# Kernel optimization log

Hardware: AMD Instinct MI355X
Metric: run time of the kernel (lower is better)

The kernel has to match this reference:

```python
import jax, jax.numpy as jnp
import numpy as np

EPS = 1e-5

def layer_norm(x, alpha, beta):
    mean = jnp.mean(x, axis=-1, keepdims=True)
    var = jnp.mean(jnp.square(x - mean), axis=-1, keepdims=True)
    return alpha * ((x - mean) / jnp.sqrt(var + EPS)) + beta

def setup_inputs() -> dict:
    key = jax.random.key(0)
    B, S, D, H = 4, 2048, 1024, 16
    Dff = 4 * D
    ks = jax.random.split(key, 8)
    inp = {
        "x": jax.random.normal(ks[0], (B, S, D), jnp.float32),
        "attention_mask": jnp.ones((B, S), jnp.int32),
        "ln1_alpha": jnp.ones((D,), jnp.float32),
        "ln1_beta": jnp.zeros((D,), jnp.float32),
        "ln2_alpha": jnp.ones((D,), jnp.float32),
        "ln2_beta": jnp.zeros((D,), jnp.float32),
        "Wq": jax.random.normal(ks[1], (D, D), jnp.float32) * 0.05,
        "Wk": jax.random.normal(ks[2], (D, D), jnp.float32) * 0.05,
        "Wv": jax.random.normal(ks[3], (D, D), jnp.float32) * 0.05,
        "Wo": jax.random.normal(ks[4], (D, D), jnp.float32) * 0.05,
        "W1": jax.random.normal(ks[5], (D, Dff), jnp.float32) * 0.02,
        "b1": jnp.zeros((Dff,), jnp.float32),
        "W2": jax.random.normal(ks[6], (Dff, D), jnp.float32) * 0.02,
        "b2": jnp.zeros((D,), jnp.float32),
    }
    return inp

def reference(x, attention_mask, ln1_alpha, ln1_beta, ln2_alpha, ln2_beta,
              Wq, Wk, Wv, Wo, W1, b1, W2, b2):
    B, S, D = x.shape
    H = 16
    dh = D // H

    # LN1 + self-attention
    y = layer_norm(x, ln1_alpha, ln1_beta)
    Q = (y @ Wq).reshape(B, S, H, dh).transpose(0, 2, 1, 3)  # [B,H,S,dh]
    K = (y @ Wk).reshape(B, S, H, dh).transpose(0, 2, 1, 3)
    V = (y @ Wv).reshape(B, S, H, dh).transpose(0, 2, 1, 3)

    scores = jnp.einsum("bhqd,bhkd->bhqk", Q, K) / jnp.sqrt(jnp.float32(dh))
    causal = jnp.tril(jnp.ones((S, S), jnp.float32))  # [S,S]
    tmask = attention_mask.astype(jnp.float32)  # [B,S]
    amask = causal[None, None, :, :] * tmask[:, None, None, :] * tmask[:, None, :, None]
    scores = jnp.where(amask > 0, scores, jnp.float32(-1e30))
    attn = jax.nn.softmax(scores, axis=-1)
    # dropout omitted (deterministic inference)
    ctx = jnp.einsum("bhqk,bhkd->bhqd", attn, V)
    ctx = ctx.transpose(0, 2, 1, 3).reshape(B, S, D)
    x = x + ctx @ Wo

    # LN2 + GELU FFN
    y = layer_norm(x, ln2_alpha, ln2_beta)
    h = jax.nn.gelu(y @ W1 + b1, approximate=False)
    x = x + (h @ W2 + b2)
    return x
```

## Files before the change

### kernel.cpp

```cpp
#include <hip/hip_runtime.h>
#include <math.h>

typedef unsigned short u16;
typedef unsigned int u32;
typedef __attribute__((ext_vector_type(4))) unsigned short u16x4;
typedef __attribute__((ext_vector_type(8))) short bf16x8;
typedef __attribute__((ext_vector_type(4))) float f32x4;

#define B_ 4
#define S_ 2048
#define D_ 1024
#define H_ 16
#define NT (B_*S_)
#define DFF 4096

static __device__ __forceinline__ float bf2f(u16 u) {
    return __uint_as_float(((u32)u) << 16);
}
static __device__ __forceinline__ u16 f2bf(float f) {
    u32 u = __float_as_uint(f);
    u32 r = (u + 0x7fffu + ((u >> 16) & 1u)) >> 16;
    return (u16)r;
}
static __device__ __forceinline__ void gload_lds16(const void* g, void* l) {
    __builtin_amdgcn_global_load_lds(
        (const __attribute__((address_space(1))) void*)g,
        (__attribute__((address_space(3))) void*)l, 16, 0, 0);
}
static __device__ __forceinline__ float gelu_fast(float x) {
    float x2 = x * x;
    float u = x * fmaf(0.044715f, x2, 1.0f);
    float e = exp2f(2.3022079f * u);
    float r = __builtin_amdgcn_rcpf(e + 1.0f);
    return x - x * r;
}

#define MBAR() do { asm volatile("" ::: "memory"); \
                    __builtin_amdgcn_s_barrier(); \
                    asm volatile("" ::: "memory"); } while (0)
#define SBAR0() __builtin_amdgcn_sched_barrier(0)

__global__ void transpose_f2b4(const float* __restrict__ s0, const float* __restrict__ s1,
                               const float* __restrict__ s2, const float* __restrict__ s3,
                               u16* __restrict__ d0, u16* __restrict__ d1,
                               u16* __restrict__ d2, u16* __restrict__ d3,
                               int R, int C) {
    const float* in = s0; u16* out = d0;
    if (blockIdx.z == 1) { in = s1; out = d1; }
    else if (blockIdx.z == 2) { in = s2; out = d2; }
    else if (blockIdx.z == 3) { in = s3; out = d3; }
    __shared__ float t[32][33];
    int c0 = blockIdx.x * 32, r0 = blockIdx.y * 32;
    int x = threadIdx.x, y = threadIdx.y;
    #pragma unroll
    for (int i = 0; i < 4; i++)
        t[y + i*8][x] = in[(long)(r0 + y + i*8) * C + c0 + x];
    __syncthreads();
    #pragma unroll
    for (int i = 0; i < 4; i++)
        out[(long)(c0 + y + i*8) * R + r0 + x] = f2bf(t[x][y + i*8]);
}

__global__ void transpose_f2b(const float* __restrict__ in, u16* __restrict__ out,
                              int R, int C) {
    __shared__ float t[32][33];
    int c0 = blockIdx.x * 32, r0 = blockIdx.y * 32;
    int x = threadIdx.x, y = threadIdx.y;
    #pragma unroll
    for (int i = 0; i < 4; i++)
        t[y + i*8][x] = in[(long)(r0 + y + i*8) * C + c0 + x];
    __syncthreads();
    #pragma unroll
    for (int i = 0; i < 4; i++)
        out[(long)(c0 + y + i*8) * R + r0 + x] = f2bf(t[x][y + i*8]);
}

__global__ void transpose_v(const u16* __restrict__ V, u16* __restrict__ Vt) {
    __shared__ u16 t[32][33];
    int z = blockIdx.z; int b = z >> 4, h = z & 15;
    int s0 = blockIdx.x * 32, d0 = blockIdx.y * 32;
    int x = threadIdx.x, y = threadIdx.y;
    const u16* in = V + ((long)b * S_ + s0) * D_ + h * 64 + d0;
    #pragma unroll
    for (int i = 0; i < 4; i++)
        t[y + i*8][x] = in[(long)(y + i*8) * D_ + x];
    __syncthreads();
    u16* out = Vt + ((long)z * 64 + d0) * S_ + s0;
    #pragma unroll
    for (int i = 0; i < 4; i++)
        out[(long)(y + i*8) * S_ + x] = t[x][y + i*8];
}

__global__ __launch_bounds__(256) void ln_kernel(
    const float* __restrict__ X, const float* __restrict__ alpha,
    const float* __restrict__ beta, u16* __restrict__ Y) {
    int row = blockIdx.x, tid = threadIdx.x;
    float4 xv = ((const float4*)(X + (long)row * D_))[tid];
    float v[4] = {xv.x, xv.y, xv.z, xv.w};
    float s = 0.f, ss = 0.f;
    #pragma unroll
    for (int i = 0; i < 4; i++) { s += v[i]; ss += v[i]*v[i]; }
    #pragma unroll
    for (int off = 32; off >= 1; off >>= 1) {
        s += __shfl_xor(s, off);
        ss += __shfl_xor(ss, off);
    }
    __shared__ float red[8];
    __shared__ float stats[2];
    int w = tid >> 6;
    if ((tid & 63) == 0) { red[w] = s; red[4 + w] = ss; }
    __syncthreads();
    if (tid == 0) {
        float S = red[0] + red[1] + red[2] + red[3];
        float SS = red[4] + red[5] + red[6] + red[7];
        float mean = S * (1.f / D_);
        float var = SS * (1.f / D_) - mean * mean;
        stats[0] = mean; stats[1] = rsqrtf(var + 1e-5f);
    }
    __syncthreads();
    float mean = stats[0], rstd = stats[1];
    float4 av = ((const float4*)alpha)[tid];
    float4 bv = ((const float4*)beta)[tid];
    u16x4 o;
    o[0] = f2bf((v[0] - mean) * rstd * av.x + bv.x);
    o[1] = f2bf((v[1] - mean) * rstd * av.y + bv.y);
    o[2] = f2bf((v[2] - mean) * rstd * av.z + bv.z);
    o[3] = f2bf((v[3] - mean) * rstd * av.w + bv.w);
    *(u16x4*)(Y + (long)row * D_ + tid * 4) = o;
}

#define BM2 256
#define BN2 256
#define BK2 64

__global__ __launch_bounds__(512, 2) void gemm8p(
    const u16* __restrict__ A, const u16* __restrict__ Bt,
    u16* __restrict__ C0, u16* __restrict__ C1, u16* __restrict__ C2,
    int N, int K, int mode, const float* __restrict__ bias) {
    __shared__ __align__(16) u16 lds[2 * 32768];

    int tid = threadIdx.x;
    int lane = tid & 63, wave = tid >> 6;
    int l15 = lane & 15, quad = lane >> 4;
    int wm = wave & 1, wn = wave >> 1;
    long tm0 = (long)blockIdx.y * BM2, tn0 = (long)blockIdx.x * BN2;
    int srow = lane >> 3;
    int scolw = ((lane & 7) ^ srow) * 8;
    int sk = l15 & 7;
    int ca0 = ((quad) ^ sk) * 8;
    int ca1 = ((4 + quad) ^ sk) * 8;
    int steps = K >> 6;

    auto STAGE = [&](int kt, int half, int buf) {
        long kk = (long)kt * BK2;
        #pragma unroll
        for (int c = 0; c < 2; c++) {
            int chunk = wave * 2 + c;
            int rloc = (half & 1) * 128 + chunk * 8 + srow;
            const u16* g = (half < 2)
                ? &A [(tm0 + rloc) * (long)K + kk + scolw]
                : &Bt[(tn0 + rloc) * (long)K + kk + scolw];
            u16* l = &lds[buf * 32768 + (half >= 2 ? 16384 : 0)
                          + (half & 1) * 8192 + chunk * 512];
            gload_lds16(g, l);
        }
    };

    f32x4 acc[8][4] = {};
    bf16x8 af[4][2], bl[2][2], bh[2][2];

    STAGE(0, 0, 0); STAGE(0, 1, 0); STAGE(0, 2, 0); STAGE(0, 3, 0);
    if (steps > 1) { STAGE(1, 2, 1); STAGE(1, 3, 1); }
    if (steps > 1) asm volatile("s_waitcnt vmcnt(4)" ::: "memory");
    else           asm volatile("s_waitcnt vmcnt(0)" ::: "memory");
    MBAR();

    for (int t = 0; t < steps; ++t) {
        int cur = t & 1;
        const u16* Ab = &lds[cur * 32768];
        const u16* Bb = &lds[cur * 32768 + 16384];
        bool pf1 = (t + 1 < steps), pf2 = (t + 2 < steps);

        #pragma unroll
        for (int mt = 0; mt < 4; mt++) {
            int row = wm*128 + mt*16 + l15;
            af[mt][0] = *(const bf16x8*)&Ab[row * BK2 + ca0];
            af[mt][1] = *(const bf16x8*)&Ab[row * BK2 + ca1];
        }
        #pragma unroll
        for (int nt = 0; nt < 2; nt++) {
            int row = wn*64 + nt*16 + l15;
            bl[nt][0] = *(const bf16x8*)&Bb[row * BK2 + ca0];
            bl[nt][1] = *(const bf16x8*)&Bb[row * BK2 + ca1];
        }
        if (pf1) STAGE(t + 1, 0, cur ^ 1);
        MBAR();
        SBAR0();
        __builtin_amdgcn_s_setprio(1);
        #pragma unroll
        for (int mt = 0; mt < 4; mt++)
            #pragma unroll
            for (int nt = 0; nt < 2; nt++) {
                acc[mt][nt] = __builtin_amdgcn_mfma_f32_16x16x32_bf16(af[mt][0], bl[nt][0], acc[mt][nt], 0,0,0);
                acc[mt][nt] = __builtin_amdgcn_mfma_f32_16x16x32_bf16(af[mt][1], bl[nt][1], acc[mt][nt], 0,0,0);
            }
        __builtin_amdgcn_s_setprio(0);
        SBAR0();
        MBAR();

        #pragma unroll
        for (int nt = 0; nt < 2; nt++) {
            int row = wn*64 + (2+nt)*16 + l15;
            bh[nt][0] = *(const bf16x8*)&Bb[row * BK2 + ca0];
            bh[nt][1] = *(const bf16x8*)&Bb[row * BK2 + ca1];
        }
        if (pf1) STAGE(t + 1, 1, cur ^ 1);
        MBAR();
        SBAR0();
        __builtin_amdgcn_s_setprio(1);
        #pragma unroll
        for (int mt = 0; mt < 4; mt++)
            #pragma unroll
            for (int nt = 0; nt < 2; nt++) {
                acc[mt][2+nt] = __builtin_amdgcn_mfma_f32_16x16x32_bf16(af[mt][0], bh[nt][0], acc[mt][2+nt], 0,0,0);
                acc[mt][2+nt] = __builtin_amdgcn_mfma_f32_16x16x32_bf16(af[mt][1], bh[nt][1], acc[mt][2+nt], 0,0,0);
            }
        __builtin_amdgcn_s_setprio(0);
        SBAR0();
        MBAR();

        #pragma unroll
        for (int mt = 0; mt < 4; mt++) {
            int row = wm*128 + 64 + mt*16 + l15;
            af[mt][0] = *(const bf16x8*)&Ab[row * BK2 + ca0];
            af[mt][1] = *(const bf16x8*)&Ab[row * BK2 + ca1];
        }
        if (pf2) STAGE(t + 2, 2, cur);
        MBAR();
        SBAR0();
        __builtin_amdgcn_s_setprio(1);
        #pragma unroll
        for (int mt = 0; mt < 4; mt++)
            #pragma unroll
            for (int nt = 0; nt < 2; nt++) {
                acc[4+mt][2+nt] = __builtin_amdgcn_mfma_f32_16x16x32_bf16(af[mt][0], bh[nt][0], acc[4+mt][2+nt], 0,0,0);
                acc[4+mt][2+nt] = __builtin_amdgcn_mfma_f32_16x16x32_bf16(af[mt][1], bh[nt][1], acc[4+mt][2+nt], 0,0,0);
            }
        __builtin_amdgcn_s_setprio(0);
        SBAR0();
        MBAR();

        if (pf2) STAGE(t + 2, 3, cur);
        MBAR();
        SBAR0();
        __builtin_amdgcn_s_setprio(1);
        #pragma unroll
        for (int mt = 0; mt < 4; mt++)
            #pragma unroll
            for (int nt = 0; nt < 2; nt++) {
                acc[4+mt][nt] = __builtin_amdgcn_mfma_f32_16x16x32_bf16(af[mt][0], bl[nt][0], acc[4+mt][nt], 0,0,0);
                acc[4+mt][nt] = __builtin_amdgcn_mfma_f32_16x16x32_bf16(af[mt][1], bl[nt][1], acc[4+mt][nt], 0,0,0);
            }
        __builtin_amdgcn_s_setprio(0);
        SBAR0();
        if (pf2) asm volatile("s_waitcnt vmcnt(4)" ::: "memory");
        else     asm volatile("s_waitcnt vmcnt(0)" ::: "memory");
        MBAR();
    }

    #pragma unroll
    for (int mt = 0; mt < 8; mt++) {
        #pragma unroll
        for (int nt = 0; nt < 4; nt++) {
            #pragma unroll
            for (int i = 0; i < 4; i++) {
                long r = tm0 + wm*128 + mt*16 + quad*4 + i;
                int cn = (int)tn0 + wn*64 + nt*16 + l15;
                float val = acc[mt][nt][i];
                if (mode == 0) {
                    int mi = cn >> 10;
                    int col = cn & 1023;
                    u16* base = (mi == 0) ? C0 : (mi == 1 ? C1 : C2);
                    base[r * 1024 + col] = f2bf(val);
                } else {
                    val += bias[cn];
                    C0[r * (long)N + cn] = f2bf(gelu_fast(val));
                }
            }
        }
    }
}

__global__ __launch_bounds__(512, 2) void gemm8p_n128(
    const u16* __restrict__ A, const u16* __restrict__ Bt,
    float* __restrict__ C, int N, int K,
    const float* __restrict__ bias, const float* __restrict__ resid) {
    __shared__ __align__(16) u16 lds[2 * 24576];

    int tid = threadIdx.x;
    int lane = tid & 63, wave = tid >> 6;
    int l15 = lane & 15, quad = lane >> 4;
    int wm = wave & 1, wn = wave >> 1;
    long tm0 = (long)blockIdx.y * 256, tn0 = (long)blockIdx.x * 128;
    int srow = lane >> 3;
    int scolw = ((lane & 7) ^ srow) * 8;
    int sk = l15 & 7;
    int ca0 = ((quad) ^ sk) * 8;
    int ca1 = ((4 + quad) ^ sk) * 8;
    int steps = K >> 6;

    auto STAGE = [&](int kt, int half, int buf) {
        long kk = (long)kt * 64;
        if (half < 2) {
            #pragma unroll
            for (int c = 0; c < 2; c++) {
                int chunk = wave * 2 + c;
                int rloc = half * 128 + chunk * 8 + srow;
                gload_lds16(&A[(tm0 + rloc) * (long)K + kk + scolw],
                            &lds[buf * 24576 + half * 8192 + chunk * 512]);
            }
        } else {
            int rloc = (half - 2) * 64 + wave * 8 + srow;
            gload_lds16(&Bt[(tn0 + rloc) * (long)K + kk + scolw],
                        &lds[buf * 24576 + 16384 + (half - 2) * 4096 + wave * 512]);
        }
    };

    f32x4 acc[8][2] = {};
    bf16x8 af[4][2], bl[2], bh[2];

    STAGE(0, 0, 0); STAGE(0, 1, 0); STAGE(0, 2, 0); STAGE(0, 3, 0);
    if (steps > 1) { STAGE(1, 2, 1); STAGE(1, 3, 1); }
    if (steps > 1) asm volatile("s_waitcnt vmcnt(2)" ::: "memory");
    else           asm volatile("s_waitcnt vmcnt(0)" ::: "memory");
    MBAR();

    for (int t = 0; t < steps; ++t) {
        int cur = t & 1;
        const u16* Ab = &lds[cur * 24576];
        const u16* Bb = &lds[cur * 24576 + 16384];
        bool pf1 = (t + 1 < steps), pf2 = (t + 2 < steps);

        #pragma unroll
        for (int mt = 0; mt < 4; mt++) {
            int row = wm*128 + mt*16 + l15;
            af[mt][0] = *(const bf16x8*)&Ab[row * 64 + ca0];
            af[mt][1] = *(const bf16x8*)&Ab[row * 64 + ca1];
        }
        {
            int row = wn*32 + l15;
            bl[0] = *(const bf16x8*)&Bb[row * 64 + ca0];
            bl[1] = *(const bf16x8*)&Bb[row * 64 + ca1];
        }
        if (pf1) STAGE(t + 1, 0, cur ^ 1);
        MBAR();
        SBAR0();
        __builtin_amdgcn_s_setprio(1);
        #pragma unroll
        for (int mt = 0; mt < 4; mt++) {
            acc[mt][0] = __builtin_amdgcn_mfma_f32_16x16x32_bf16(af[mt][0], bl[0], acc[mt][0], 0,0,0);
            acc[mt][0] = __builtin_amdgcn_mfma_f32_16x16x32_bf16(af[mt][1], bl[1], acc[mt][0], 0,0,0);
        }
        __builtin_amdgcn_s_setprio(0);
        SBAR0();
        MBAR();

        {
            int row = wn*32 + 16 + l15;
            bh[0] = *(const bf16x8*)&Bb[row * 64 + ca0];
            bh[1] = *(const bf16x8*)&Bb[row * 64 + ca1];
        }
        if (pf1) STAGE(t + 1, 1, cur ^ 1);
        MBAR();
        SBAR0();
        __builtin_amdgcn_s_setprio(1);
        #pragma unroll
        for (int mt = 0; mt < 4; mt++) {
            acc[mt][1] = __builtin_amdgcn_mfma_f32_16x16x32_bf16(af[mt][0], bh[0], acc[mt][1], 0,0,0);
            acc[mt][1] = __builtin_amdgcn_mfma_f32_16x16x32_bf16(af[mt][1], bh[1], acc[mt][1], 0,0,0);
        }
        __builtin_amdgcn_s_setprio(0);
        SBAR0();
        MBAR();

        #pragma unroll
        for (int mt = 0; mt < 4; mt++) {
            int row = wm*128 + 64 + mt*16 + l15;
            af[mt][0] = *(const bf16x8*)&Ab[row * 64 + ca0];
            af[mt][1] = *(const bf16x8*)&Ab[row * 64 + ca1];
        }
        if (pf2) STAGE(t + 2, 2, cur);
        MBAR();
        SBAR0();
        __builtin_amdgcn_s_setprio(1);
        #pragma unroll
        for (int mt = 0; mt < 4; mt++) {
            acc[4+mt][1] = __builtin_amdgcn_mfma_f32_16x16x32_bf16(af[mt][0], bh[0], acc[4+mt][1], 0,0,0);
            acc[4+mt][1] = __builtin_amdgcn_mfma_f32_16x16x32_bf16(af[mt][1], bh[1], acc[4+mt][1], 0,0,0);
        }
        __builtin_amdgcn_s_setprio(0);
        SBAR0();
        MBAR();

        if (pf2) STAGE(t + 2, 3, cur);
        MBAR();
        SBAR0();
        __builtin_amdgcn_s_setprio(1);
        #pragma unroll
        for (int mt = 0; mt < 4; mt++) {
            acc[4+mt][0] = __builtin_amdgcn_mfma_f32_16x16x32_bf16(af[mt][0], bl[0], acc[4+mt][0], 0,0,0);
            acc[4+mt][0] = __builtin_amdgcn_mfma_f32_16x16x32_bf16(af[mt][1], bl[1], acc[4+mt][0], 0,0,0);
        }
        __builtin_amdgcn_s_setprio(0);
        SBAR0();
        if (pf2) asm volatile("s_waitcnt vmcnt(2)" ::: "memory");
        else     asm volatile("s_waitcnt vmcnt(0)" ::: "memory");
        MBAR();
    }

    #pragma unroll
    for (int mt = 0; mt < 8; mt++) {
        #pragma unroll
        for (int nt = 0; nt < 2; nt++) {
            #pragma unroll
            for (int i = 0; i < 4; i++) {
                long r = tm0 + wm*128 + mt*16 + quad*4 + i;
                int cn = (int)tn0 + wn*32 + nt*16 + l15;
                long idx = r * (long)N + cn;
                float bb = bias ? bias[cn] : 0.0f;
                C[idx] = acc[mt][nt][i] + bb + resid[idx];
            }
        }
    }
}

#define LDP 72

__global__ __launch_bounds__(128, 2) void attn_kernel(
    const u16* __restrict__ Q, const u16* __restrict__ Kg, const u16* __restrict__ Vt,
    const int* __restrict__ mask, u16* __restrict__ O) {
    __shared__ __align__(16) u16 Psm[2][32 * LDP];
    int tid = threadIdx.x;
    int lane = tid & 63, wave = tid >> 6;
    int l15 = lane & 15, quad = lane >> 4;
    int bh = blockIdx.x; int b = bh >> 4, h = bh & 15;
    int j = blockIdx.y * 2 + wave;
    long tokBase = (long)b * S_;
    const float SCL = 0.125f * 1.4426950408889634f;
    const float MMAX = 20.0f;

    const bf16x8 ones = {16256,16256,16256,16256,16256,16256,16256,16256};
    u16* Pw = Psm[wave];
    const int* mb = mask + b * S_;

    #pragma unroll
    for (int half = 0; half < 2; half++) {
        int t = half ? (63 - j) : j;
        int q0 = t * 32;

        bf16x8 aq[2][2];
        #pragma unroll
        for (int mt = 0; mt < 2; mt++) {
            const u16* qptr = Q + (tokBase + q0 + mt*16 + l15) * D_ + h * 64;
            aq[mt][0] = *(const bf16x8*)(qptr + quad * 8);
            aq[mt][1] = *(const bf16x8*)(qptr + 32 + quad * 8);
        }

        f32x4 o[2][4] = {};
        f32x4 lacc[2] = {};
        int ktiles = t / 2 + 1;

        bf16x8 kb[4][2];
        #pragma unroll
        for (int nt = 0; nt < 4; nt++) {
            const u16* kp = Kg + (tokBase + nt*16 + l15) * D_ + h * 64;
            kb[nt][0] = *(const bf16x8*)(kp + quad * 8);
            kb[nt][1] = *(const bf16x8*)(kp + 32 + quad * 8);
        }

        for (int kt = 0; kt < ktiles; kt++) {
            int k0 = kt * 64;
            bf16x8 vb[4][2];
            #pragma unroll
            for (int d = 0; d < 4; d++) {
                const u16* vp = Vt + ((long)bh * 64 + d*16 + l15) * S_ + k0;
                vb[d][0] = *(const bf16x8*)(vp + quad * 8);
                vb[d][1] = *(const bf16x8*)(vp + 32 + quad * 8);
            }

            f32x4 s[2][4] = {};
            #pragma unroll
            for (int nt = 0; nt < 4; nt++) {
                s[0][nt] = __builtin_amdgcn_mfma_f32_16x16x32_bf16(aq[0][0], kb[nt][0], s[0][nt], 0,0,0);
                s[0][nt] = __builtin_amdgcn_mfma_f32_16x16x32_bf16(aq[0][1], kb[nt][1], s[0][nt], 0,0,0);
                s[1][nt] = __builtin_amdgcn_mfma_f32_16x16x32_bf16(aq[1][0], kb[nt][0], s[1][nt], 0,0,0);
                s[1][nt] = __builtin_amdgcn_mfma_f32_16x16x32_bf16(aq[1][1], kb[nt][1], s[1][nt], 0,0,0);
            }

            int k1 = (kt + 1 < ktiles) ? k0 + 64 : k0;
            bf16x8 kbn[4][2];
            #pragma unroll
            for (int nt = 0; nt < 4; nt++) {
                const u16* kp = Kg + (tokBase + k1 + nt*16 + l15) * D_ + h * 64;
                kbn[nt][0] = *(const bf16x8*)(kp + quad * 8);
                kbn[nt][1] = *(const bf16x8*)(kp + 32 + quad * 8);
            }

            int mk = 0;
            #pragma unroll
            for (int nt = 0; nt < 4; nt++)
                if (mb[k0 + nt*16 + l15] != 0) mk |= (1 << nt);

            #pragma unroll
            for (int mt = 0; mt < 2; mt++) {
                #pragma unroll
                for (int i = 0; i < 4; i++) {
                    int qq = q0 + mt*16 + quad*4 + i;
                    #pragma unroll
                    for (int nt = 0; nt < 4; nt++) {
                        int kc = k0 + nt*16 + l15;
                        float p = exp2f(fmaf(s[mt][nt][i], SCL, -MMAX));
                        p = (kc <= qq && ((mk >> nt) & 1)) ? p : 0.f;
                        Pw[(mt*16 + quad*4 + i) * LDP + nt*16 + l15] = f2bf(p);
                    }
                }
            }
            asm volatile("s_waitcnt lgkmcnt(0)" ::: "memory");

            #pragma unroll
            for (int hv = 0; hv < 2; hv++) {
                bf16x8 ap0 = *(const bf16x8*)&Pw[l15 * LDP + hv*32 + quad*8];
                bf16x8 ap1 = *(const bf16x8*)&Pw[(16 + l15) * LDP + hv*32 + quad*8];
                #pragma unroll
                for (int d = 0; d < 4; d++) {
                    o[0][d] = __builtin_amdgcn_mfma_f32_16x16x32_bf16(ap0, vb[d][hv], o[0][d], 0,0,0);
                    o[1][d] = __builtin_amdgcn_mfma_f32_16x16x32_bf16(ap1, vb[d][hv], o[1][d], 0,0,0);
                }
                lacc[0] = __builtin_amdgcn_mfma_f32_16x16x32_bf16(ap0, ones, lacc[0], 0,0,0);
                lacc[1] = __builtin_amdgcn_mfma_f32_16x16x32_bf16(ap1, ones, lacc[1], 0,0,0);
            }

            #pragma unroll
            for (int nt = 0; nt < 4; nt++) {
                kb[nt][0] = kbn[nt][0];
                kb[nt][1] = kbn[nt][1];
            }
        }

        #pragma unroll
        for (int mt = 0; mt < 2; mt++) {
            #pragma unroll
            for (int i = 0; i < 4; i++) {
                float inv = 1.f / lacc[mt][i];
                long r = tokBase + q0 + mt*16 + quad*4 + i;
                #pragma unroll
                for (int d = 0; d < 4; d++)
                    O[r * D_ + h*64 + d*16 + l15] = f2bf(o[mt][d][i] * inv);
            }
        }
    }
}

extern "C" void kernel_launch(void* const* d_in, const int* in_sizes, int n_in,
                              void* d_out, int out_size, void* d_ws, size_t ws_size,
                              hipStream_t stream) {
    const float* x    = (const float*)d_in[0];
    const int*   am   = (const int*)d_in[1];
    const float* ln1a = (const float*)d_in[2];
    const float* ln1b = (const float*)d_in[3];
    const float* ln2a = (const float*)d_in[4];
    const float* ln2b = (const float*)d_in[5];
    const float* wq   = (const float*)d_in[6];
    const float* wk   = (const float*)d_in[7];
    const float* wv   = (const float*)d_in[8];
    const float* wo   = (const float*)d_in[9];
    const float* w1   = (const float*)d_in[10];
    const float* b1   = (const float*)d_in[11];
    const float* w2   = (const float*)d_in[12];
    const float* b2   = (const float*)d_in[13];
    float* out = (float*)d_out;

    char* ws = (char*)d_ws;
    const size_t MB16 = (size_t)16 * 1024 * 1024;
    u16* y1      = (u16*)(ws + 0 * MB16);
    u16* q       = (u16*)(ws + 1 * MB16);
    u16* k       = (u16*)(ws + 2 * MB16);
    u16* v       = (u16*)(ws + 3 * MB16);
    u16* wqt     = (u16*)(ws + 4 * MB16 + 0 * (size_t)D_ * D_ * 2);
    u16* wkt     = (u16*)(ws + 4 * MB16 + 1 * (size_t)D_ * D_ * 2);
    u16* wvt     = (u16*)(ws + 4 * MB16 + 2 * (size_t)D_ * D_ * 2);
    u16* wot     = (u16*)(ws + 4 * MB16 + 3 * (size_t)D_ * D_ * 2);
    u16* y2      = y1;
    u16* w1t     = q;
    u16* w2t     = q + (size_t)D_ * DFF;
    u16* h_full  = k;
    u16* ctx     = v;
    u16*   vt  = (u16*)d_out;
    float* x1f = out;

    dim3 tb(32, 8);
    transpose_f2b4<<<dim3(D_/32, D_/32, 4), tb, 0, stream>>>(
        wq, wk, wv, wo, wqt, wkt, wvt, wot, D_, D_);

    ln_kernel<<<NT, 256, 0, stream>>>(x, ln1a, ln1b, y1);

    gemm8p<<<dim3(3*D_/BN2, NT/BM2), 512, 0, stream>>>(
        y1, wqt, q, k, v, 3*D_, D_, 0, nullptr);

    transpose_v<<<dim3(S_/32, 2, B_*H_), tb, 0, stream>>>(v, vt);

    attn_kernel<<<dim3(B_*H_, 16), 128, 0, stream>>>(q, k, vt, am, ctx);

    gemm8p_n128<<<dim3(D_/128, NT/256), 512, 0, stream>>>(
        ctx, wot, x1f, D_, D_, nullptr, x);

    transpose_f2b<<<dim3(DFF/32, D_/32), tb, 0, stream>>>(w1, w1t, D_, DFF);
    transpose_f2b<<<dim3(D_/32, DFF/32), tb, 0, stream>>>(w2, w2t, DFF, D_);

    ln_kernel<<<NT, 256, 0, stream>>>(x1f, ln2a, ln2b, y2);

    gemm8p<<<dim3(DFF/BN2, NT/BM2), 512, 0, stream>>>(
        y2, w1t, h_full, h_full, h_full, DFF, D_, 2, b1);

    gemm8p_n128<<<dim3(D_/128, NT/256), 512, 0, stream>>>(
        h_full, w2t, out, D_, DFF, b2, x1f);
}
```

Before: 605.6 us.

## Keep attention probabilities in registers via transposed MFMA and lane shuffles

The attention kernel now computes S transposed (K as the A operand), so each lane holds probabilities for a single query row. These are packed to bf16 with v_cvt_pk_bf16_f32 and regrouped with shuffles to form the P operand of the PV MFMA directly, which removes the LDS round trip and its wait. The row sum is now accumulated in VALU and reduced with shuffles instead of an extra MFMA against a ones vector. Masks come from a single ballot, and the output is written as 4-wide vector stores. This adds shuffle and select work and changes the bf16 rounding path for P.

```diff
diff --git a/kernel.cpp b/kernel.cpp
--- a/kernel.cpp
+++ b/kernel.cpp
@@ -21,6 +21,11 @@
     u32 u = __float_as_uint(f);
     u32 r = (u + 0x7fffu + ((u >> 16) & 1u)) >> 16;
     return (u16)r;
+}
+static __device__ __forceinline__ u32 cvtpk(float lo, float hi) {
+    u32 r;
+    asm("v_cvt_pk_bf16_f32 %0, %1, %2" : "=v"(r) : "v"(lo), "v"(hi));
+    return r;
 }
 static __device__ __forceinline__ void gload_lds16(const void* g, void* l) {
     __builtin_amdgcn_global_load_lds(
@@ -434,12 +439,9 @@
     }
 }
 
-#define LDP 72
-
 __global__ __launch_bounds__(128, 2) void attn_kernel(
     const u16* __restrict__ Q, const u16* __restrict__ Kg, const u16* __restrict__ Vt,
     const int* __restrict__ mask, u16* __restrict__ O) {
-    __shared__ __align__(16) u16 Psm[2][32 * LDP];
     int tid = threadIdx.x;
     int lane = tid & 63, wave = tid >> 6;
     int l15 = lane & 15, quad = lane >> 4;
@@ -448,10 +450,9 @@
     long tokBase = (long)b * S_;
     const float SCL = 0.125f * 1.4426950408889634f;
     const float MMAX = 20.0f;
-
-    const bf16x8 ones = {16256,16256,16256,16256,16256,16256,16256,16256};
-    u16* Pw = Psm[wave];
     const int* mb = mask + b * S_;
+
+    union U4 { u32 u[4]; bf16x8 v; };
 
     #pragma unroll
     for (int half = 0; half < 2; half++) {
@@ -467,7 +468,7 @@
         }
 
         f32x4 o[2][4] = {};
-        f32x4 lacc[2] = {};
+        float psum[2] = {0.f, 0.f};
         int ktiles = t / 2 + 1;
 
         bf16x8 kb[4][2];
@@ -491,10 +492,10 @@
             f32x4 s[2][4] = {};
             #pragma unroll
             for (int nt = 0; nt < 4; nt++) {
-                s[0][nt] = __builtin_amdgcn_mfma_f32_16x16x32_bf16(aq[0][0], kb[nt][0], s[0][nt], 0,0,0);
-                s[0][nt] = __builtin_amdgcn_mfma_f32_16x16x32_bf16(aq[0][1], kb[nt][1], s[0][nt], 0,0,0);
-                s[1][nt] = __builtin_amdgcn_mfma_f32_16x16x32_bf16(aq[1][0], kb[nt][0], s[1][nt], 0,0,0);
-                s[1][nt] = __builtin_amdgcn_mfma_f32_16x16x32_bf16(aq[1][1], kb[nt][1], s[1][nt], 0,0,0);
+                s[0][nt] = __builtin_amdgcn_mfma_f32_16x16x32_bf16(kb[nt][0], aq[0][0], s[0][nt], 0,0,0);
+                s[0][nt] = __builtin_amdgcn_mfma_f32_16x16x32_bf16(kb[nt][1], aq[0][1], s[0][nt], 0,0,0);
+                s[1][nt] = __builtin_amdgcn_mfma_f32_16x16x32_bf16(kb[nt][0], aq[1][0], s[1][nt], 0,0,0);
+                s[1][nt] = __builtin_amdgcn_mfma_f32_16x16x32_bf16(kb[nt][1], aq[1][1], s[1][nt], 0,0,0);
             }
 
             int k1 = (kt + 1 < ktiles) ? k0 + 64 : k0;
@@ -506,38 +507,53 @@
                 kbn[nt][1] = *(const bf16x8*)(kp + 32 + quad * 8);
             }
 
-            int mk = 0;
-            #pragma unroll
-            for (int nt = 0; nt < 4; nt++)
-                if (mb[k0 + nt*16 + l15] != 0) mk |= (1 << nt);
-
+            unsigned long long mv = __ballot(mb[k0 + lane] != 0);
+
+            #pragma unroll
+            for (int mt = 0; mt < 2; mt++) {
+                int qq = q0 + mt*16 + l15;
+                #pragma unroll
+                for (int nt = 0; nt < 4; nt++) {
+                    #pragma unroll
+                    for (int i = 0; i < 4; i++) {
+                        int kloc = nt*16 + quad*4 + i;
+                        float p = exp2f(fmaf(s[mt][nt][i], SCL, -MMAX));
+                        bool ok = (k0 + kloc <= qq) && ((mv >> kloc) & 1ull);
+                        p = ok ? p : 0.f;
+                        s[mt][nt][i] = p;
+                        psum[mt] += p;
+                    }
+                }
+            }
+
+            bool lo = (quad < 2);
+            int srcA = ((quad & 1) << 1) * 16 + l15;
             #pragma unroll
             for (int mt = 0; mt < 2; mt++) {
                 #pragma unroll
-                for (int i = 0; i < 4; i++) {
-                    int qq = q0 + mt*16 + quad*4 + i;
+                for (int hv = 0; hv < 2; hv++) {
+                    u32 x0 = cvtpk(s[mt][2*hv][0],   s[mt][2*hv][1]);
+                    u32 x1 = cvtpk(s[mt][2*hv][2],   s[mt][2*hv][3]);
+                    u32 y0 = cvtpk(s[mt][2*hv+1][0], s[mt][2*hv+1][1]);
+                    u32 y1 = cvtpk(s[mt][2*hv+1][2], s[mt][2*hv+1][3]);
+                    u32 gx0 = (u32)__shfl((int)x0, srcA);
+                    u32 gy0 = (u32)__shfl((int)y0, srcA);
+                    u32 gx1 = (u32)__shfl((int)x1, srcA);
+                    u32 gy1 = (u32)__shfl((int)y1, srcA);
+                    u32 gx2 = (u32)__shfl((int)x0, srcA + 16);
+                    u32 gy2 = (u32)__shfl((int)y0, srcA + 16);
+                    u32 gx3 = (u32)__shfl((int)x1, srcA + 16);
+                    u32 gy3 = (u32)__shfl((int)y1, srcA + 16);
+                    U4 pu;
+                    pu.u[0] = lo ? gx0 : gy0;
+                    pu.u[1] = lo ? gx1 : gy1;
+                    pu.u[2] = lo ? gx2 : gy2;
+                    pu.u[3] = lo ? gx3 : gy3;
                     #pragma unroll
-                    for (int nt = 0; nt < 4; nt++) {
-                        int kc = k0 + nt*16 + l15;
-                        float p = exp2f(fmaf(s[mt][nt][i], SCL, -MMAX));
-                        p = (kc <= qq && ((mk >> nt) & 1)) ? p : 0.f;
-                        Pw[(mt*16 + quad*4 + i) * LDP + nt*16 + l15] = f2bf(p);
-                    }
+                    for (int d = 0; d < 4; d++)
+                        o[mt][d] = __builtin_amdgcn_mfma_f32_16x16x32_bf16(
+                            vb[d][hv], pu.v, o[mt][d], 0,0,0);
                 }
-            }
-            asm volatile("s_waitcnt lgkmcnt(0)" ::: "memory");
-
-            #pragma unroll
-            for (int hv = 0; hv < 2; hv++) {
-                bf16x8 ap0 = *(const bf16x8*)&Pw[l15 * LDP + hv*32 + quad*8];
-                bf16x8 ap1 = *(const bf16x8*)&Pw[(16 + l15) * LDP + hv*32 + quad*8];
-                #pragma unroll
-                for (int d = 0; d < 4; d++) {
-                    o[0][d] = __builtin_amdgcn_mfma_f32_16x16x32_bf16(ap0, vb[d][hv], o[0][d], 0,0,0);
-                    o[1][d] = __builtin_amdgcn_mfma_f32_16x16x32_bf16(ap1, vb[d][hv], o[1][d], 0,0,0);
-                }
-                lacc[0] = __builtin_amdgcn_mfma_f32_16x16x32_bf16(ap0, ones, lacc[0], 0,0,0);
-                lacc[1] = __builtin_amdgcn_mfma_f32_16x16x32_bf16(ap1, ones, lacc[1], 0,0,0);
             }
 
             #pragma unroll
@@ -549,13 +565,18 @@
 
         #pragma unroll
         for (int mt = 0; mt < 2; mt++) {
-            #pragma unroll
-            for (int i = 0; i < 4; i++) {
-                float inv = 1.f / lacc[mt][i];
-                long r = tokBase + q0 + mt*16 + quad*4 + i;
+            float ps = psum[mt];
+            ps += __shfl_xor(ps, 16);
+            ps += __shfl_xor(ps, 32);
+            float inv = 1.f / ps;
+            long r = tokBase + q0 + mt*16 + l15;
+            #pragma unroll
+            for (int d = 0; d < 4; d++) {
+                u16x4 ov;
                 #pragma unroll
-                for (int d = 0; d < 4; d++)
-                    O[r * D_ + h*64 + d*16 + l15] = f2bf(o[mt][d][i] * inv);
+                for (int i = 0; i < 4; i++)
+                    ov[i] = f2bf(o[mt][d][i] * inv);
+                *(u16x4*)(O + r * D_ + h*64 + d*16 + quad*4) = ov;
             }
         }
     }
```

Result: no change. 605.2 us (-0.1%).
